# Optimization experiments

Hardware: AMD Instinct MI355X
Metric: run time of the kernel (lower is better)

The kernel has to match this reference:

```python
import jax, jax.numpy as jnp
import numpy as np

S, B, T = 512, 512, 64

def setup_inputs() -> dict:
    key = jax.random.key(0)
    k1, k2, k3, k4, k5 = jax.random.split(key, 5)
    feats = jax.random.normal(k1, (S, B, T), dtype=jnp.float32)
    # contiguous-prefix masks with variable lengths in [S//2, S]
    lengths = jax.random.randint(k2, (B,), S // 2, S + 1)
    mask = (jnp.arange(S)[None, :] < lengths[:, None]).astype(jnp.float32)  # (B,S)
    u = lambda k, shp: jax.random.uniform(k, shp, jnp.float32, -0.1, 0.1)
    return {
        "feats": feats,
        "mask": mask,
        "start_transitions": u(k3, (T,)),
        "end_transitions": u(k4, (T,)),
        "transitions": u(k5, (T, T)),
    }

def reference(feats, mask, start_transitions, end_transitions, transitions):
    # feats: (S, B, T) emissions; mask: (B, S) 1/0 float, left-aligned
    s, b, t = feats.shape
    maskT = mask.T  # (S, B)

    score0 = start_transitions[None, :] + feats[0]  # (B, T)

    def step(vscore, inp):
        emis, m = inp  # (B,T), (B,)
        # score[b, i, j] = vscore[b,i] + trans[i,j] + emis[b,j]
        scores = vscore[:, :, None] + transitions[None, :, :] + emis[:, None, :]
        best = jnp.max(scores, axis=1)                       # (B, T)
        bp = jnp.argmax(scores, axis=1).astype(jnp.int32)    # (B, T) backpointers
        m1 = m[:, None]
        new_v = best * m1 + vscore * (1.0 - m1)
        return new_v, bp * m1.astype(jnp.int32)

    final_v, history = jax.lax.scan(step, score0, (feats[1:], maskT[1:]))
    final_v = final_v + end_transitions[None, :]
    last_path = jnp.argmax(final_v, axis=1).astype(jnp.int32)  # (B,)

    # append pad row of zeros -> history: (S, B, T)
    history = jnp.concatenate([history, jnp.zeros((1, b, t), jnp.int32)], axis=0)

    # insert last_path at position (length - 1) for every tag column
    lengths = jnp.sum(mask, axis=1).astype(jnp.int32)  # (B,)
    hb = history.transpose(1, 0, 2)                    # (B, S, T)
    hb = hb.at[jnp.arange(b), lengths - 1, :].set(last_path[:, None])
    history = hb.transpose(1, 0, 2)                    # (S, B, T)

    # backtrack: decode_idx[i] = history[i][b, last_path[b]], i = S-2 .. 0
    def back(lp, h):
        new = jnp.take_along_axis(h, lp[:, None], axis=1)[:, 0]
        return new, new

    _, dec = jax.lax.scan(back, last_path, history[:-1], reverse=True)  # (S-1, B)
    # decode_idx[S-1] is uninitialized in the torch code; fill with argmax last tag
    decode = jnp.concatenate([dec, last_path[None, :]], axis=0)  # (S, B)
    return decode.T  # (B, S)
```

## Files before the change

kernel.cpp:

```cpp
#include <hip/hip_runtime.h>

#define SS 512
#define BB 512
#define TT 64
#define NTHREADS 256
#define FSTRIDE ((size_t)BB * TT)

template <int CTRL>
__device__ __forceinline__ float dppf(float x) {
    return __int_as_float(__builtin_amdgcn_mov_dpp(__float_as_int(x), CTRL, 0xF, 0xF, true));
}
template <int CTRL>
__device__ __forceinline__ int dppi(int x) {
    return __builtin_amdgcn_mov_dpp(x, CTRL, 0xF, 0xF, true);
}

__global__ __launch_bounds__(NTHREADS) void viterbi_fused(
    const float* __restrict__ feats,
    const float* __restrict__ mask,
    const float* __restrict__ startt,
    const float* __restrict__ endt,
    const float* __restrict__ trans,
    int* __restrict__ out)
{
    __shared__ float vbuf[2][TT];
    __shared__ unsigned char hist[SS - 1][TT];
    __shared__ float redbuf[4];
    __shared__ int lenSh;

    const int b   = blockIdx.x;
    const int tid = threadIdx.x;
    const int j   = tid >> 2;
    const int li  = tid & 3;
    const int base_i = li * 16;
    const int wid = tid >> 6;
    const int lane = tid & 63;

    float msum = mask[b * SS + tid] + mask[b * SS + 256 + tid];
#pragma unroll
    for (int off = 1; off < 64; off <<= 1) msum += __shfl_xor(msum, off);
    if (lane == 0) redbuf[wid] = msum;
    __syncthreads();
    if (tid == 0) {
        float t = redbuf[0] + redbuf[1] + redbuf[2] + redbuf[3];
        lenSh = (int)(t + 0.5f);
    }

    float tcr[16];
#pragma unroll
    for (int k = 0; k < 16; ++k) tcr[k] = trans[(base_i + k) * TT + j];

    if (tid < TT) vbuf[0][tid] = startt[tid] + feats[(size_t)b * TT + tid];
    __syncthreads();

    const int len = lenSh;
    int p = 0;

    const float* fb = feats + (size_t)b * TT + j;
    float e0 = fb[1 * FSTRIDE];
    float e1 = fb[2 * FSTRIDE];

    for (int s = 1; s < len; ++s) {
        int sn = s + 2; if (sn > SS - 1) sn = SS - 1;
        float e_pre = fb[(size_t)sn * FSTRIDE];

        float v[16];
#pragma unroll
        for (int q = 0; q < 4; ++q) {
            float4 t4 = *(const float4*)&vbuf[p][base_i + q * 4];
            v[q * 4 + 0] = t4.x; v[q * 4 + 1] = t4.y;
            v[q * 4 + 2] = t4.z; v[q * 4 + 3] = t4.w;
        }

        float sc[16];
#pragma unroll
        for (int k = 0; k < 16; ++k) sc[k] = (v[k] + tcr[k]) + e0;

        float c0 = sc[0];  int x0 = 0;
        float c1 = sc[4];  int x1 = 4;
        float c2 = sc[8];  int x2 = 8;
        float c3 = sc[12]; int x3 = 12;
#pragma unroll
        for (int k = 1; k < 4; ++k) {
            if (sc[k]      > c0) { c0 = sc[k];      x0 = k; }
            if (sc[4 + k]  > c1) { c1 = sc[4 + k];  x1 = 4 + k; }
            if (sc[8 + k]  > c2) { c2 = sc[8 + k];  x2 = 8 + k; }
            if (sc[12 + k] > c3) { c3 = sc[12 + k]; x3 = 12 + k; }
        }
        if (c1 > c0) { c0 = c1; x0 = x1; }
        if (c3 > c2) { c2 = c3; x2 = x3; }
        if (c2 > c0) { c0 = c2; x0 = x2; }
        float best = c0;
        int   bi   = base_i + x0;

        {
            float ov = dppf<0xB1>(best);
            int   oi = dppi<0xB1>(bi);
            if (ov > best || (ov == best && oi < bi)) { best = ov; bi = oi; }
            ov = dppf<0x4E>(best);
            oi = dppi<0x4E>(bi);
            if (ov > best || (ov == best && oi < bi)) { best = ov; bi = oi; }
        }

        if (li == 0) {
            vbuf[p ^ 1][j] = best;
            hist[s - 1][j] = (unsigned char)bi;
        }
        __syncthreads();
        p ^= 1;
        e0 = e1;
        e1 = e_pre;
    }

    if (tid < TT) {
        float fv = vbuf[p][tid] + endt[tid];
        int bix = tid;
#pragma unroll
        for (int off = 1; off < 64; off <<= 1) {
            float ov = __shfl_xor(fv, off);
            int   oi = __shfl_xor(bix, off);
            if (ov > fv || (ov == fv && oi < bix)) { fv = ov; bix = oi; }
        }
        if (tid == 0) {
            int* ob = out + (size_t)b * SS;
            int cur = bix;
            ob[SS - 1] = cur;
            ob[len - 1] = cur;
            for (int s2 = len - 2; s2 >= 0; --s2) {
                cur = hist[s2][cur];
                ob[s2] = cur;
            }
        }
    }

    for (int s2 = len + tid; s2 < SS - 1; s2 += NTHREADS)
        out[(size_t)b * SS + s2] = 0;
}

extern "C" void kernel_launch(void* const* d_in, const int* in_sizes, int n_in,
                              void* d_out, int out_size, void* d_ws, size_t ws_size,
                              hipStream_t stream) {
    const float* feats  = (const float*)d_in[0];
    const float* mask   = (const float*)d_in[1];
    const float* startt = (const float*)d_in[2];
    const float* endt   = (const float*)d_in[3];
    const float* trans  = (const float*)d_in[4];
    int* out = (int*)d_out;

    viterbi_fused<<<dim3(BB), dim3(NTHREADS), 0, stream>>>(
        feats, mask, startt, endt, trans, out);
}
```

Measured before the change: 260.9 us.

## Batch emission prefetch by 8 steps and use lightweight LDS-only barrier

Restructures the Viterbi recurrence loop to prefetch emissions for the next 8 time steps in registers while the current 8 are processed, replacing the single-step rolling prefetch. Replaces __syncthreads with a raw s_waitcnt lgkmcnt(0) + s_barrier so outstanding global loads are not waited on at each step barrier. Also moves transition/initial loads before the mask reduction to overlap latency. Increases register use and relies on the inline asm barrier being sufficient for LDS ordering.

```diff
diff --git a/kernel.cpp b/kernel.cpp
--- a/kernel.cpp
+++ b/kernel.cpp
@@ -13,6 +13,10 @@
 template <int CTRL>
 __device__ __forceinline__ int dppi(int x) {
     return __builtin_amdgcn_mov_dpp(x, CTRL, 0xF, 0xF, true);
+}
+
+__device__ __forceinline__ void barrier_lgkm() {
+    asm volatile("s_waitcnt lgkmcnt(0)\n\ts_barrier" ::: "memory");
 }
 
 __global__ __launch_bounds__(NTHREADS) void viterbi_fused(
@@ -36,6 +40,12 @@
     const int wid = tid >> 6;
     const int lane = tid & 63;
 
+    float tcr[16];
+#pragma unroll
+    for (int k = 0; k < 16; ++k) tcr[k] = trans[(base_i + k) * TT + j];
+
+    if (tid < TT) vbuf[0][tid] = startt[tid] + feats[(size_t)b * TT + tid];
+
     float msum = mask[b * SS + tid] + mask[b * SS + 256 + tid];
 #pragma unroll
     for (int off = 1; off < 64; off <<= 1) msum += __shfl_xor(msum, off);
@@ -45,25 +55,14 @@
         float t = redbuf[0] + redbuf[1] + redbuf[2] + redbuf[3];
         lenSh = (int)(t + 0.5f);
     }
-
-    float tcr[16];
-#pragma unroll
-    for (int k = 0; k < 16; ++k) tcr[k] = trans[(base_i + k) * TT + j];
-
-    if (tid < TT) vbuf[0][tid] = startt[tid] + feats[(size_t)b * TT + tid];
     __syncthreads();
 
     const int len = lenSh;
     int p = 0;
 
     const float* fb = feats + (size_t)b * TT + j;
-    float e0 = fb[1 * FSTRIDE];
-    float e1 = fb[2 * FSTRIDE];
 
-    for (int s = 1; s < len; ++s) {
-        int sn = s + 2; if (sn > SS - 1) sn = SS - 1;
-        float e_pre = fb[(size_t)sn * FSTRIDE];
-
+    auto body = [&](float e, int s) {
         float v[16];
 #pragma unroll
         for (int q = 0; q < 4; ++q) {
@@ -71,10 +70,9 @@
             v[q * 4 + 0] = t4.x; v[q * 4 + 1] = t4.y;
             v[q * 4 + 2] = t4.z; v[q * 4 + 3] = t4.w;
         }
-
         float sc[16];
 #pragma unroll
-        for (int k = 0; k < 16; ++k) sc[k] = (v[k] + tcr[k]) + e0;
+        for (int k = 0; k < 16; ++k) sc[k] = (v[k] + tcr[k]) + e;
 
         float c0 = sc[0];  int x0 = 0;
         float c1 = sc[4];  int x1 = 4;
@@ -106,10 +104,33 @@
             vbuf[p ^ 1][j] = best;
             hist[s - 1][j] = (unsigned char)bi;
         }
-        __syncthreads();
+        barrier_lgkm();
         p ^= 1;
-        e0 = e1;
-        e1 = e_pre;
+    };
+
+    float ec[8], en[8];
+#pragma unroll
+    for (int u = 0; u < 8; ++u) {
+        int sn = 1 + u; if (sn > SS - 1) sn = SS - 1;
+        ec[u] = fb[(size_t)sn * FSTRIDE];
+    }
+
+    int s = 1;
+    while (s + 8 <= len) {
+#pragma unroll
+        for (int u = 0; u < 8; ++u) {
+            int sn = s + 8 + u; if (sn > SS - 1) sn = SS - 1;
+            en[u] = fb[(size_t)sn * FSTRIDE];
+        }
+#pragma unroll
+        for (int u = 0; u < 8; ++u) body(ec[u], s + u);
+#pragma unroll
+        for (int u = 0; u < 8; ++u) ec[u] = en[u];
+        s += 8;
+    }
+#pragma unroll
+    for (int u = 0; u < 7; ++u) {
+        if (s + u < len) body(ec[u], s + u);
     }
 
     if (tid < TT) {
```

After: 255.8 us. No clear change (-2.0%).
